# Kernel optimization log

Hardware: AMD Instinct MI355X
Metric: run time of the kernel (lower is better)

The kernel has to match this reference:

```python
import jax, jax.numpy as jnp
import numpy as np
from jax import lax

B, T, L = 2048, 80, 128


def setup_inputs() -> dict:
    key = jax.random.key(0)
    k1, k2, k3, k4, k5 = jax.random.split(key, 5)
    x = jax.random.normal(k1, (B, T, L), dtype=jnp.float32)  # emissions (model logits)
    y = jax.random.randint(k2, (B, T), 0, L)                 # gold tag sequence
    trans = jax.random.normal(k3, (L, L), dtype=jnp.float32) * 0.1
    start_trans = jax.random.normal(k4, (L,), dtype=jnp.float32) * 0.1
    end_trans = jax.random.normal(k5, (L,), dtype=jnp.float32) * 0.1
    return {"x": x, "trans": trans, "start_trans": start_trans,
            "end_trans": end_trans, "y": y}


def reference(x, trans, start_trans, end_trans, y):
    # Linear-chain CRF log-likelihood (TorchCRF semantics, mask = all ones).
    # x: [B,T,L] emissions, y: [B,T] gold tags. Returns [B] log-likelihoods.
    # --- numerator: score of the gold path ---
    emit = jnp.take_along_axis(x, y[..., None], axis=2).squeeze(-1).sum(axis=1)  # [B]
    tr = trans[y[:, :-1], y[:, 1:]].sum(axis=1)                                  # [B]
    numerator = start_trans[y[:, 0]] + emit + tr + end_trans[y[:, -1]]           # [B]
    # --- denominator: log-partition via forward algorithm (scan over time) ---
    alpha0 = start_trans[None, :] + x[:, 0]  # [B,L]
    xt = jnp.swapaxes(x, 0, 1)[1:]           # [T-1,B,L]

    def step(alpha, h_t):
        # alpha[b,i] + trans[i,j] -> logsumexp over i, then add emission h_t[b,j]
        a = jax.nn.logsumexp(alpha[:, :, None] + trans[None, :, :], axis=1) + h_t
        return a, None

    alpha, _ = lax.scan(step, alpha0, xt)
    log_z = jax.nn.logsumexp(alpha + end_trans[None, :], axis=1)  # [B]
    return numerator - log_z
```

## Files before the change

kernel.cpp:

```cpp
#include <hip/hip_runtime.h>
#include <math.h>


#define CRF_B 2048
#define CRF_T 80
#define CRF_L 128

typedef __attribute__((ext_vector_type(8))) short bf16x8_t;
typedef __attribute__((ext_vector_type(4))) float f32x4_t;

__device__ __forceinline__ short f2bf(float f) {
    unsigned u = __float_as_uint(f);
    unsigned r = (u + 0x7FFF + ((u >> 16) & 1)) >> 16;
    return (short)r;
}

__global__ __launch_bounds__(256) void crf_mfma_kernel(
    const float* __restrict__ x,
    const float* __restrict__ trans,
    const float* __restrict__ start_trans,
    const float* __restrict__ end_trans,
    const int*   __restrict__ y,
    float* __restrict__ out)
{
    const int b0   = blockIdx.x * 8;
    const int tid  = threadIdx.x;
    const int w    = tid >> 6;
    const int lane = tid & 63;
    const int quad = lane >> 4;
    const int n16  = lane & 15;

    __shared__ __attribute__((aligned(16))) short Vb[2][16][136];
    __shared__ __attribute__((aligned(16))) float maxbuf[16][4];
    __shared__ float numbuf[8];

    {
        const int rr = tid >> 5, tt = tid & 31;
        const int bb = b0 + rr;
        const int* yb = y + bb * CRF_T;
        const float* xbn = x + (size_t)bb * CRF_T * CRF_L;
        float p = 0.f;
        for (int t = tt; t < CRF_T; t += 32) {
            const int yt = yb[t];
            p += xbn[t * CRF_L + yt];
            if (t + 1 < CRF_T) p += trans[yt * CRF_L + yb[t + 1]];
            else               p += end_trans[yt];
            if (t == 0)        p += start_trans[yt];
        }
        p += __shfl_xor(p, 1);  p += __shfl_xor(p, 2);  p += __shfl_xor(p, 4);
        p += __shfl_xor(p, 8);  p += __shfl_xor(p, 16);
        if (tt == 0) numbuf[rr] = p;
    }

    bf16x8_t Bf[2][4];
    int   cols[2];
    float expend[2], stc[2];
    #pragma unroll
    for (int c2 = 0; c2 < 2; ++c2) {
        const int col = 32 * w + 16 * c2 + n16;
        cols[c2]   = col;
        expend[c2] = __expf(end_trans[col]);
        stc[c2]    = start_trans[col];
        #pragma unroll
        for (int kk = 0; kk < 4; ++kk) {
            union { bf16x8_t v; short s[8]; } u;
            #pragma unroll
            for (int j = 0; j < 8; ++j) {
                const int k = 32 * kk + quad * 8 + j;
                u.s[j] = f2bf(__expf(trans[k * CRF_L + col]));
            }
            Bf[c2][kk] = u.v;
        }
    }

    const float* xrow[4];
    #pragma unroll
    for (int r = 0; r < 4; ++r)
        xrow[r] = x + (size_t)(b0 + ((quad * 4 + r) & 7)) * CRF_T * CRF_L;

    float crun[4] = {0.f, 0.f, 0.f, 0.f};
    float invM[4] = {1.f, 1.f, 1.f, 1.f};
    f32x4_t P[2];

    float xa[2][4], xb[2][4];
    #pragma unroll
    for (int c2 = 0; c2 < 2; ++c2)
    #pragma unroll
    for (int r = 0; r < 4; ++r)
        xa[c2][r] = xrow[r][cols[c2]];

    auto body = [&](int t, float (&xc)[2][4], float (&xn)[2][4]) {
        if (t + 1 < CRF_T) {
            #pragma unroll
            for (int c2 = 0; c2 < 2; ++c2)
            #pragma unroll
            for (int r = 0; r < 4; ++r)
                xn[c2][r] = xrow[r][(t + 1) * CRF_L + cols[c2]];
        }
        const int cur = t & 1, prv = cur ^ 1;

        if (t == 0) {
            #pragma unroll
            for (int c2 = 0; c2 < 2; ++c2) {
                #pragma unroll
                for (int r = 0; r < 4; ++r)
                    P[c2][r] = __expf(stc[c2] + xc[c2][r]);
            }
        } else {
            bf16x8_t Af[4];
            #pragma unroll
            for (int kk = 0; kk < 4; ++kk)
                Af[kk] = *(const bf16x8_t*)&Vb[prv][n16][32 * kk + quad * 8];
            #pragma unroll
            for (int c2 = 0; c2 < 2; ++c2) {
                f32x4_t acc = {0.f, 0.f, 0.f, 0.f};
                #pragma unroll
                for (int kk = 0; kk < 4; ++kk)
                    acc = __builtin_amdgcn_mfma_f32_16x16x32_bf16(Af[kk], Bf[c2][kk], acc, 0, 0, 0);
                #pragma unroll
                for (int r = 0; r < 4; ++r)
                    P[c2][r] = acc[r] * __expf(xc[c2][r]) * invM[r];
            }
        }

        const bool renorm = ((t & 3) == 3) && (t < CRF_T - 1);
        if (renorm) {
            #pragma unroll
            for (int r = 0; r < 4; ++r) {
                float m = fmaxf(P[0][r], P[1][r]);
                m = fmaxf(m, __shfl_xor(m, 1));
                m = fmaxf(m, __shfl_xor(m, 2));
                m = fmaxf(m, __shfl_xor(m, 4));
                m = fmaxf(m, __shfl_xor(m, 8));
                if (n16 == 0) maxbuf[quad * 4 + r][w] = m;
            }
        }

        #pragma unroll
        for (int c2 = 0; c2 < 2; ++c2)
        #pragma unroll
        for (int r = 0; r < 4; ++r)
            Vb[cur][quad * 4 + r][cols[c2]] = f2bf(P[c2][r]);

        __syncthreads();

        if (renorm) {
            #pragma unroll
            for (int r = 0; r < 4; ++r) {
                const f32x4_t mb = *(const f32x4_t*)&maxbuf[quad * 4 + r][0];
                const float M = fmaxf(fmaxf(mb[0], mb[1]), fmaxf(mb[2], mb[3]));
                crun[r] += __logf(M);
                invM[r]  = 1.f / M;
            }
        } else {
            #pragma unroll
            for (int r = 0; r < 4; ++r) invM[r] = 1.f;
        }
    };

    for (int t = 0; t < CRF_T; t += 2) {
        body(t,     xa, xb);
        body(t + 1, xb, xa);
    }

    #pragma unroll
    for (int r = 0; r < 4; ++r) {
        float v = P[0][r] * expend[0] + P[1][r] * expend[1];
        v += __shfl_xor(v, 1); v += __shfl_xor(v, 2);
        v += __shfl_xor(v, 4); v += __shfl_xor(v, 8);
        if (n16 == 0) maxbuf[quad * 4 + r][w] = v;
    }
    __syncthreads();
    if (w == 0 && n16 == 0 && quad < 2) {
        #pragma unroll
        for (int r = 0; r < 4; ++r) {
            const int row = quad * 4 + r;
            const f32x4_t sb = *(const f32x4_t*)&maxbuf[row][0];
            const float S = sb[0] + sb[1] + sb[2] + sb[3];
            out[b0 + row] = numbuf[row] - (crun[r] + __logf(S));
        }
    }
}

extern "C" void kernel_launch(void* const* d_in, const int* in_sizes, int n_in,
                              void* d_out, int out_size, void* d_ws, size_t ws_size,
                              hipStream_t stream) {
    const float* x     = (const float*)d_in[0];
    const float* trans = (const float*)d_in[1];
    const float* st    = (const float*)d_in[2];
    const float* et    = (const float*)d_in[3];
    const int*   y     = (const int*)d_in[4];
    float* out = (float*)d_out;

    crf_mfma_kernel<<<CRF_B / 8, 256, 0, stream>>>(x, trans, st, et, y, out);
}
```

Baseline: 178.9 us.

## Process 16 sequences per block with transposed MFMA and per-step renormalization

Each block now handles 16 batch rows instead of 8, filling the MFMA's 16-wide dimension that was previously half duplicated, and halves the grid. The matmul is transposed so exp(trans) is the A operand and each lane owns one sequence row, which allows vectorized float4 emission loads and packed bf16 stores to LDS. Renormalization now happens every step, with a cheap max reduction using double-buffered max storage, and bf16 conversion switches from round-to-nearest to truncation. Truncation may add slight bias to the log-partition, and there are half as many blocks to fill the GPU.

```diff
diff --git a/kernel.cpp b/kernel.cpp
--- a/kernel.cpp
+++ b/kernel.cpp
@@ -9,13 +9,11 @@
 typedef __attribute__((ext_vector_type(8))) short bf16x8_t;
 typedef __attribute__((ext_vector_type(4))) float f32x4_t;
 
-__device__ __forceinline__ short f2bf(float f) {
-    unsigned u = __float_as_uint(f);
-    unsigned r = (u + 0x7FFF + ((u >> 16) & 1)) >> 16;
-    return (short)r;
+__device__ __forceinline__ int pack_bf16_trunc(float lo, float hi) {
+    return (int)((__float_as_uint(lo) >> 16) | (__float_as_uint(hi) & 0xFFFF0000u));
 }
 
-__global__ __launch_bounds__(256) void crf_mfma_kernel(
+__global__ __launch_bounds__(256) void crf_v3_kernel(
     const float* __restrict__ x,
     const float* __restrict__ trans,
     const float* __restrict__ start_trans,
@@ -23,162 +21,146 @@
     const int*   __restrict__ y,
     float* __restrict__ out)
 {
-    const int b0   = blockIdx.x * 8;
     const int tid  = threadIdx.x;
     const int w    = tid >> 6;
     const int lane = tid & 63;
     const int quad = lane >> 4;
     const int n16  = lane & 15;
+    const int row0 = blockIdx.x * 16;
 
     __shared__ __attribute__((aligned(16))) short Vb[2][16][136];
-    __shared__ __attribute__((aligned(16))) float maxbuf[16][4];
-    __shared__ float numbuf[8];
+    __shared__ __attribute__((aligned(16))) float maxb[2][16][4];
+    __shared__ __attribute__((aligned(16))) float sumb[16][4];
+    __shared__ float numb[16];
 
     {
-        const int rr = tid >> 5, tt = tid & 31;
-        const int bb = b0 + rr;
+        const int rr = tid >> 4, tt = tid & 15;
+        const int bb = row0 + rr;
         const int* yb = y + bb * CRF_T;
         const float* xbn = x + (size_t)bb * CRF_T * CRF_L;
         float p = 0.f;
-        for (int t = tt; t < CRF_T; t += 32) {
+        for (int t = tt; t < CRF_T; t += 16) {
             const int yt = yb[t];
             p += xbn[t * CRF_L + yt];
-            if (t + 1 < CRF_T) p += trans[yt * CRF_L + yb[t + 1]];
-            else               p += end_trans[yt];
-            if (t == 0)        p += start_trans[yt];
+            p += (t + 1 < CRF_T) ? trans[yt * CRF_L + yb[t + 1]] : end_trans[yt];
+            if (t == 0) p += start_trans[yt];
         }
-        p += __shfl_xor(p, 1);  p += __shfl_xor(p, 2);  p += __shfl_xor(p, 4);
-        p += __shfl_xor(p, 8);  p += __shfl_xor(p, 16);
-        if (tt == 0) numbuf[rr] = p;
+        p += __shfl_xor(p, 1); p += __shfl_xor(p, 2);
+        p += __shfl_xor(p, 4); p += __shfl_xor(p, 8);
+        if (tt == 0) numb[rr] = p;
     }
 
-    bf16x8_t Bf[2][4];
-    int   cols[2];
-    float expend[2], stc[2];
+    bf16x8_t Af[2][4];
     #pragma unroll
-    for (int c2 = 0; c2 < 2; ++c2) {
-        const int col = 32 * w + 16 * c2 + n16;
-        cols[c2]   = col;
-        expend[c2] = __expf(end_trans[col]);
-        stc[c2]    = start_trans[col];
+    for (int mt = 0; mt < 2; ++mt) {
+        const int m = 32 * w + 16 * mt + n16;
         #pragma unroll
         for (int kk = 0; kk < 4; ++kk) {
             union { bf16x8_t v; short s[8]; } u;
             #pragma unroll
             for (int j = 0; j < 8; ++j) {
-                const int k = 32 * kk + quad * 8 + j;
-                u.s[j] = f2bf(__expf(trans[k * CRF_L + col]));
+                const int k = 32 * kk + 8 * quad + j;
+                const float e = __expf(trans[k * CRF_L + m]);
+                u.s[j] = (short)(__float_as_uint(e) >> 16);
             }
-            Bf[c2][kk] = u.v;
+            Af[mt][kk] = u.v;
         }
     }
 
-    const float* xrow[4];
-    #pragma unroll
-    for (int r = 0; r < 4; ++r)
-        xrow[r] = x + (size_t)(b0 + ((quad * 4 + r) & 7)) * CRF_T * CRF_L;
+    const int sc0 = 32 * w + 4 * quad;
+    const int sc1 = sc0 + 16;
+    const float* xr = x + (size_t)(row0 + n16) * CRF_T * CRF_L;
 
-    float crun[4] = {0.f, 0.f, 0.f, 0.f};
-    float invM[4] = {1.f, 1.f, 1.f, 1.f};
+    f32x4_t ex_end[2], st4[2];
+    {
+        const f32x4_t e0 = *(const f32x4_t*)&end_trans[sc0];
+        const f32x4_t e1 = *(const f32x4_t*)&end_trans[sc1];
+        #pragma unroll
+        for (int r = 0; r < 4; ++r) {
+            ex_end[0][r] = __expf(e0[r]);
+            ex_end[1][r] = __expf(e1[r]);
+        }
+        st4[0] = *(const f32x4_t*)&start_trans[sc0];
+        st4[1] = *(const f32x4_t*)&start_trans[sc1];
+    }
+
     f32x4_t P[2];
+    float invM = 1.f, crun = 0.f;
+    f32x4_t xc[2], xn[2];
+    xc[0] = *(const f32x4_t*)&xr[sc0];
+    xc[1] = *(const f32x4_t*)&xr[sc1];
 
-    float xa[2][4], xb[2][4];
-    #pragma unroll
-    for (int c2 = 0; c2 < 2; ++c2)
-    #pragma unroll
-    for (int r = 0; r < 4; ++r)
-        xa[c2][r] = xrow[r][cols[c2]];
-
-    auto body = [&](int t, float (&xc)[2][4], float (&xn)[2][4]) {
+    for (int t = 0; t < CRF_T; ++t) {
         if (t + 1 < CRF_T) {
-            #pragma unroll
-            for (int c2 = 0; c2 < 2; ++c2)
-            #pragma unroll
-            for (int r = 0; r < 4; ++r)
-                xn[c2][r] = xrow[r][(t + 1) * CRF_L + cols[c2]];
+            xn[0] = *(const f32x4_t*)&xr[(t + 1) * CRF_L + sc0];
+            xn[1] = *(const f32x4_t*)&xr[(t + 1) * CRF_L + sc1];
         }
-        const int cur = t & 1, prv = cur ^ 1;
 
         if (t == 0) {
             #pragma unroll
-            for (int c2 = 0; c2 < 2; ++c2) {
-                #pragma unroll
-                for (int r = 0; r < 4; ++r)
-                    P[c2][r] = __expf(stc[c2] + xc[c2][r]);
+            for (int r = 0; r < 4; ++r) {
+                P[0][r] = __expf(st4[0][r] + xc[0][r]);
+                P[1][r] = __expf(st4[1][r] + xc[1][r]);
             }
         } else {
-            bf16x8_t Af[4];
+            const short* vrow = &Vb[(t - 1) & 1][n16][0];
+            bf16x8_t Bf[4];
             #pragma unroll
             for (int kk = 0; kk < 4; ++kk)
-                Af[kk] = *(const bf16x8_t*)&Vb[prv][n16][32 * kk + quad * 8];
+                Bf[kk] = *(const bf16x8_t*)&vrow[32 * kk + 8 * quad];
             #pragma unroll
-            for (int c2 = 0; c2 < 2; ++c2) {
+            for (int mt = 0; mt < 2; ++mt) {
                 f32x4_t acc = {0.f, 0.f, 0.f, 0.f};
                 #pragma unroll
                 for (int kk = 0; kk < 4; ++kk)
-                    acc = __builtin_amdgcn_mfma_f32_16x16x32_bf16(Af[kk], Bf[c2][kk], acc, 0, 0, 0);
+                    acc = __builtin_amdgcn_mfma_f32_16x16x32_bf16(Af[mt][kk], Bf[kk], acc, 0, 0, 0);
                 #pragma unroll
                 for (int r = 0; r < 4; ++r)
-                    P[c2][r] = acc[r] * __expf(xc[c2][r]) * invM[r];
+                    P[mt][r] = acc[r] * __expf(xc[mt][r]) * invM;
             }
         }
 
-        const bool renorm = ((t & 3) == 3) && (t < CRF_T - 1);
-        if (renorm) {
-            #pragma unroll
-            for (int r = 0; r < 4; ++r) {
-                float m = fmaxf(P[0][r], P[1][r]);
-                m = fmaxf(m, __shfl_xor(m, 1));
-                m = fmaxf(m, __shfl_xor(m, 2));
-                m = fmaxf(m, __shfl_xor(m, 4));
-                m = fmaxf(m, __shfl_xor(m, 8));
-                if (n16 == 0) maxbuf[quad * 4 + r][w] = m;
-            }
+        if (t < CRF_T - 1) {
+            float g = fmaxf(fmaxf(fmaxf(P[0][0], P[0][1]), fmaxf(P[0][2], P[0][3])),
+                            fmaxf(fmaxf(P[1][0], P[1][1]), fmaxf(P[1][2], P[1][3])));
+            g = fmaxf(g, __shfl_xor(g, 16));
+            g = fmaxf(g, __shfl_xor(g, 32));
+            if (lane < 16) maxb[t & 1][n16][w] = g;
+
+            short* dst = &Vb[t & 1][n16][0];
+            const int d00 = pack_bf16_trunc(P[0][0], P[0][1]);
+            const int d01 = pack_bf16_trunc(P[0][2], P[0][3]);
+            const int d10 = pack_bf16_trunc(P[1][0], P[1][1]);
+            const int d11 = pack_bf16_trunc(P[1][2], P[1][3]);
+            *(int2*)&dst[sc0] = make_int2(d00, d01);
+            *(int2*)&dst[sc1] = make_int2(d10, d11);
+
+            __syncthreads();
+
+            const f32x4_t mb = *(const f32x4_t*)&maxb[t & 1][n16][0];
+            const float M = fmaxf(fmaxf(mb[0], mb[1]), fmaxf(mb[2], mb[3]));
+            crun += __logf(M);
+            invM = __builtin_amdgcn_rcpf(M);
         }
 
-        #pragma unroll
-        for (int c2 = 0; c2 < 2; ++c2)
-        #pragma unroll
-        for (int r = 0; r < 4; ++r)
-            Vb[cur][quad * 4 + r][cols[c2]] = f2bf(P[c2][r]);
-
-        __syncthreads();
-
-        if (renorm) {
-            #pragma unroll
-            for (int r = 0; r < 4; ++r) {
-                const f32x4_t mb = *(const f32x4_t*)&maxbuf[quad * 4 + r][0];
-                const float M = fmaxf(fmaxf(mb[0], mb[1]), fmaxf(mb[2], mb[3]));
-                crun[r] += __logf(M);
-                invM[r]  = 1.f / M;
-            }
-        } else {
-            #pragma unroll
-            for (int r = 0; r < 4; ++r) invM[r] = 1.f;
-        }
-    };
-
-    for (int t = 0; t < CRF_T; t += 2) {
-        body(t,     xa, xb);
-        body(t + 1, xb, xa);
+        xc[0] = xn[0];
+        xc[1] = xn[1];
     }
 
+    float sv = 0.f;
     #pragma unroll
-    for (int r = 0; r < 4; ++r) {
-        float v = P[0][r] * expend[0] + P[1][r] * expend[1];
-        v += __shfl_xor(v, 1); v += __shfl_xor(v, 2);
-        v += __shfl_xor(v, 4); v += __shfl_xor(v, 8);
-        if (n16 == 0) maxbuf[quad * 4 + r][w] = v;
-    }
+    for (int mt = 0; mt < 2; ++mt)
+    #pragma unroll
+    for (int r = 0; r < 4; ++r)
+        sv += P[mt][r] * ex_end[mt][r];
+    sv += __shfl_xor(sv, 16);
+    sv += __shfl_xor(sv, 32);
+    if (lane < 16) sumb[n16][w] = sv;
     __syncthreads();
-    if (w == 0 && n16 == 0 && quad < 2) {
-        #pragma unroll
-        for (int r = 0; r < 4; ++r) {
-            const int row = quad * 4 + r;
-            const f32x4_t sb = *(const f32x4_t*)&maxbuf[row][0];
-            const float S = sb[0] + sb[1] + sb[2] + sb[3];
-            out[b0 + row] = numbuf[row] - (crun[r] + __logf(S));
-        }
+    if (tid < 16) {
+        const f32x4_t sb = *(const f32x4_t*)&sumb[tid][0];
+        const float S = sb[0] + sb[1] + sb[2] + sb[3];
+        out[row0 + tid] = numb[tid] - (crun + __logf(S));
     }
 }
 
@@ -192,5 +174,5 @@
     const int*   y     = (const int*)d_in[4];
     float* out = (float*)d_out;
 
-    crf_mfma_kernel<<<CRF_B / 8, 256, 0, stream>>>(x, trans, st, et, y, out);
+    crf_v3_kernel<<<CRF_B / 16, 256, 0, stream>>>(x, trans, st, et, y, out);
 }
```

Measured after the change: 167.3 us. 1.07x faster.
